# Performance work log

Measured on AMD Instinct MI355X. Metric: run time of the kernel, lower is better.

Reference implementation:

```python
import jax, jax.numpy as jnp
import numpy as np

NUM_HEADS = 16
NUM_KV_HEADS = 4
HEAD_DIM = 128
WINDOW = 1024  # sliding window: key j visible to query i iff 0 <= i - j <= WINDOW
SCALE = 0.08838834764831845  # 1/sqrt(HEAD_DIM)
NEG_INF = -1e30


def setup_inputs() -> dict:
    key = jax.random.key(0)
    k1, k2, k3, k4 = jax.random.split(key, 4)
    B, S = 4, 2048
    T = B * S
    return {
        "q": jax.random.normal(k1, (T, NUM_HEADS * HEAD_DIM), dtype=jnp.float32),
        "k": jax.random.normal(k2, (T, NUM_KV_HEADS * HEAD_DIM), dtype=jnp.float32),
        "v": jax.random.normal(k3, (T, NUM_KV_HEADS * HEAD_DIM), dtype=jnp.float32),
        "sinks": jax.random.normal(k4, (NUM_HEADS,), dtype=jnp.float32),
        "batch": B,
        "seqlen": S,
    }


def reference(q, k, v, sinks, batch, seqlen):
    """Varlen causal sliding-window attention with learnable per-head sink logits.

    Equal-length sequences: total_tokens = batch * seqlen, matching
    cu_seqlens = [0, S, 2S, ...] in flash_attn_varlen_func.
    """
    B, S = batch, seqlen
    g = NUM_HEADS // NUM_KV_HEADS
    q = q.reshape(B, S, NUM_HEADS, HEAD_DIM)
    k = k.reshape(B, S, NUM_KV_HEADS, HEAD_DIM)
    v = v.reshape(B, S, NUM_KV_HEADS, HEAD_DIM)
    # GQA: expand kv heads to match query heads
    k = jnp.repeat(k, g, axis=2)  # [B,S,H,D]
    v = jnp.repeat(v, g, axis=2)

    logits = jnp.einsum("bqhd,bkhd->bhqk", q, k) * SCALE  # [B,H,S,S]

    i = jnp.arange(S)[:, None]
    j = jnp.arange(S)[None, :]
    mask = (j <= i) & ((i - j) <= WINDOW)  # causal + sliding window (left=WINDOW, right=-1)
    logits = jnp.where(mask, logits, NEG_INF)

    # Learnable sink: one extra virtual logit per head, contributing no value.
    sink_col = jnp.broadcast_to(sinks[None, :, None, None], (B, NUM_HEADS, S, 1))
    logits = jnp.concatenate([logits, sink_col], axis=-1)  # [B,H,S,S+1]
    probs = jax.nn.softmax(logits, axis=-1)[..., :S]  # drop sink prob (value = 0)

    o = jnp.einsum("bhqk,bkhd->bqhd", probs, v)  # [B,S,H,D]
    return o.reshape(B * S, NUM_HEADS * HEAD_DIM)
```

## Files before the change

### kernel.cpp

```cpp
#include <hip/hip_runtime.h>
#include <hip/hip_bf16.h>

#define NH    16
#define NKVH  4
#define HD    128
#define WIN   1024
#define SEQ   2048
#define NB    4
#define QROW  (NH * HD)
#define KROW  (NKVH * HD)
#define LOG2E 1.4426950408889634f
#define QSC   (0.08838834764831845f * LOG2E)

#define KSTR 136
#define VSTR 40

typedef __attribute__((ext_vector_type(8))) short short8;
typedef __attribute__((ext_vector_type(4))) float float4v;

__device__ __forceinline__ unsigned short f2bf(float f) {
    unsigned int u = __float_as_uint(f);
    unsigned int r = (u + 0x7FFFu + ((u >> 16) & 1u)) >> 16;
    return (unsigned short)r;
}

__device__ __forceinline__ unsigned int pk2bf(float a, float b) {
    float2 t; t.x = a; t.y = b;
    __hip_bfloat162 h = __float22bfloat162_rn(t);
    union { __hip_bfloat162 h; unsigned int u; } cv;
    cv.h = h;
    return cv.u;
}

__global__ __launch_bounds__(256)
void cvt_k_kernel(const float* __restrict__ kg, unsigned short* __restrict__ kb) {
    const size_t idx = ((size_t)blockIdx.x * 256 + threadIdx.x) * 8;
    float4 a = *(const float4*)(kg + idx);
    float4 b = *(const float4*)(kg + idx + 4);
    uint4 w;
    w.x = pk2bf(a.x, a.y); w.y = pk2bf(a.z, a.w);
    w.z = pk2bf(b.x, b.y); w.w = pk2bf(b.z, b.w);
    *(uint4*)(kb + idx) = w;
}

#define VTSTR 72
__global__ __launch_bounds__(256)
void cvt_vt_kernel(const float* __restrict__ vg, unsigned short* __restrict__ vt) {
    __shared__ unsigned short T[128 * VTSTR];
    const int blk = blockIdx.x;
    const int b   = blk >> 7;
    const int kvh = (blk >> 5) & 3;
    const int kb  = blk & 31;
    const int t   = threadIdx.x;

    const int klocal = t >> 2;
    const int d0     = (t & 3) * 32;
    const float* src = vg + (size_t)(b * SEQ + kb * 64 + klocal) * KROW + kvh * HD + d0;
#pragma unroll
    for (int c = 0; c < 8; ++c) {
        float4 x = *(const float4*)(src + c * 4);
        T[(d0 + c * 4 + 0) * VTSTR + klocal] = f2bf(x.x);
        T[(d0 + c * 4 + 1) * VTSTR + klocal] = f2bf(x.y);
        T[(d0 + c * 4 + 2) * VTSTR + klocal] = f2bf(x.z);
        T[(d0 + c * 4 + 3) * VTSTR + klocal] = f2bf(x.w);
    }
    __syncthreads();

    const int d    = t >> 1;
    const int half = t & 1;
    const unsigned short* s = &T[d * VTSTR + half * 32];
    unsigned short* dst = vt + ((size_t)((b * NKVH + kvh) * HD) + d) * SEQ + kb * 64 + half * 32;
#pragma unroll
    for (int c = 0; c < 4; ++c)
        *(uint4*)(dst + c * 8) = *(const uint4*)(s + c * 8);
}

__global__ __launch_bounds__(256, 3)
void attn_swa_sink_kernel(const float* __restrict__ qg,
                          const unsigned short* __restrict__ kb,
                          const unsigned short* __restrict__ vt,
                          const float* __restrict__ sinks,
                          float* __restrict__ og) {
    __shared__ __align__(16) unsigned short Klds[32 * KSTR];
    __shared__ __align__(16) unsigned short Vlds[128 * VSTR];

    const int gid  = blockIdx.x;
    const int xcd  = gid & 7;
    const int rest = gid >> 3;
    const int qt   = rest >> 1;
    const int g    = ((rest & 1) << 3) | xcd;
    const int b    = g >> 2;
    const int kvh  = g & 3;

    const int tid  = threadIdx.x;
    const int wave = tid >> 6;
    const int lane = tid & 63;
    const int l15  = lane & 15;
    const int quad = lane >> 4;
    const int h    = kvh * 4 + wave;
    const int q0   = qt * 32;

    const float* qbase = qg + (size_t)(b * SEQ) * QROW;
    const unsigned short* kbase = kb + (size_t)(b * SEQ) * KROW + kvh * HD;
    const unsigned short* vtbase = vt + (size_t)((b * NKVH + kvh) * HD) * SEQ;

    short8 qf[2][4];
#pragma unroll
    for (int qs = 0; qs < 2; ++qs) {
        const float* qr = qbase + (size_t)(q0 + qs * 16 + l15) * QROW + h * HD + quad * 8;
#pragma unroll
        for (int c = 0; c < 4; ++c) {
            float4 x = *(const float4*)(qr + c * 32);
            float4 y = *(const float4*)(qr + c * 32 + 4);
            union { unsigned int u[4]; short8 s; } cv;
            cv.u[0] = pk2bf(x.x * QSC, x.y * QSC);
            cv.u[1] = pk2bf(x.z * QSC, x.w * QSC);
            cv.u[2] = pk2bf(y.x * QSC, y.y * QSC);
            cv.u[3] = pk2bf(y.z * QSC, y.w * QSC);
            qf[qs][c] = cv.s;
        }
    }

    const float sinkv = sinks[h] * LOG2E;
    float m_i[2] = { sinkv, sinkv };
    float l_i[2] = { 1.0f, 1.0f };
    float4v accO[2][8];
#pragma unroll
    for (int qs = 0; qs < 2; ++qs)
#pragma unroll
        for (int f = 0; f < 8; ++f) accO[qs][f] = (float4v)0.0f;

    const int kr  = tid >> 3, kcg = tid & 7;
    const int lrow = ((kr & 1) << 4) | (kr >> 1);
    const int vd  = tid >> 1, vh = tid & 1;

    int kt0 = q0 - WIN; if (kt0 < 0) kt0 = 0;
    const int kend = q0 + 32;

    uint4 kpre0, kpre1, vpre0, vpre1;
    {
        const unsigned short* kp = kbase + (size_t)(kt0 + kr) * KROW + kcg * 16;
        kpre0 = *(const uint4*)(kp);
        kpre1 = *(const uint4*)(kp + 8);
        const unsigned short* vp = vtbase + (size_t)vd * SEQ + kt0 + vh * 16;
        vpre0 = *(const uint4*)(vp);
        vpre1 = *(const uint4*)(vp + 8);
    }

    for (int k0 = kt0; k0 < kend; k0 += 32) {
        __syncthreads();
        *(uint4*)&Klds[lrow * KSTR + kcg * 16]     = kpre0;
        *(uint4*)&Klds[lrow * KSTR + kcg * 16 + 8] = kpre1;
        *(uint4*)&Vlds[vd * VSTR + vh * 16]        = vpre0;
        *(uint4*)&Vlds[vd * VSTR + vh * 16 + 8]    = vpre1;
        if (k0 + 32 < kend) {
            const unsigned short* kp = kbase + (size_t)(k0 + 32 + kr) * KROW + kcg * 16;
            kpre0 = *(const uint4*)(kp);
            kpre1 = *(const uint4*)(kp + 8);
            const unsigned short* vp = vtbase + (size_t)vd * SEQ + (k0 + 32) + vh * 16;
            vpre0 = *(const uint4*)(vp);
            vpre1 = *(const uint4*)(vp + 8);
        }
        __syncthreads();

        float4v sacc[2][2];
        sacc[0][0] = (float4v)0.0f; sacc[0][1] = (float4v)0.0f;
        sacc[1][0] = (float4v)0.0f; sacc[1][1] = (float4v)0.0f;
#pragma unroll
        for (int c = 0; c < 4; ++c) {
            short8 kf0 = *(const short8*)&Klds[(l15)      * KSTR + c * 32 + quad * 8];
            short8 kf1 = *(const short8*)&Klds[(16 + l15) * KSTR + c * 32 + quad * 8];
            sacc[0][0] = __builtin_amdgcn_mfma_f32_16x16x32_bf16(kf0, qf[0][c], sacc[0][0], 0, 0, 0);
            sacc[0][1] = __builtin_amdgcn_mfma_f32_16x16x32_bf16(kf0, qf[1][c], sacc[0][1], 0, 0, 0);
            sacc[1][0] = __builtin_amdgcn_mfma_f32_16x16x32_bf16(kf1, qf[0][c], sacc[1][0], 0, 0, 0);
            sacc[1][1] = __builtin_amdgcn_mfma_f32_16x16x32_bf16(kf1, qf[1][c], sacc[1][1], 0, 0, 0);
        }

        short8 pf[2];
#pragma unroll
        for (int qs = 0; qs < 2; ++qs) {
            const int query = q0 + qs * 16 + l15;
            const bool full = (k0 + 31 <= q0 + qs * 16) && (q0 + qs * 16 + 15 - k0 <= WIN);
            float ps[2][4];
            float mx = -3.0e38f;
            if (full) {
#pragma unroll
                for (int ks = 0; ks < 2; ++ks)
#pragma unroll
                    for (int r = 0; r < 4; ++r) {
                        float s = sacc[ks][qs][r];
                        ps[ks][r] = s;
                        mx = fmaxf(mx, s);
                    }
            } else {
#pragma unroll
                for (int ks = 0; ks < 2; ++ks)
#pragma unroll
                    for (int r = 0; r < 4; ++r) {
                        const int key = k0 + 8 * quad + 2 * r + ks;
                        const unsigned d = (unsigned)(query - key);
                        float s = (d <= WIN) ? sacc[ks][qs][r] : -1.0e30f;
                        ps[ks][r] = s;
                        mx = fmaxf(mx, s);
                    }
            }
            mx = fmaxf(mx, __shfl_xor(mx, 16));
            mx = fmaxf(mx, __shfl_xor(mx, 32));
            const float mold = m_i[qs];
            const float mnew = fmaxf(mold, mx);
            m_i[qs] = mnew;
            float sum = 0.0f;
            union { unsigned int u[4]; short8 s; } cv;
#pragma unroll
            for (int r = 0; r < 4; ++r) {
                const float p0 = exp2f(ps[0][r] - mnew);
                const float p1 = exp2f(ps[1][r] - mnew);
                sum += p0 + p1;
                cv.u[r] = pk2bf(p0, p1);
            }
            pf[qs] = cv.s;
            sum += __shfl_xor(sum, 16);
            sum += __shfl_xor(sum, 32);
            if (__any(mnew > mold)) {
                const float alpha = exp2f(mold - mnew);
                l_i[qs] = l_i[qs] * alpha + sum;
#pragma unroll
                for (int r = 0; r < 4; ++r) {
                    const float ar = __shfl(alpha, quad * 4 + r);
#pragma unroll
                    for (int f = 0; f < 8; ++f) accO[qs][f][r] *= ar;
                }
            } else {
                l_i[qs] += sum;
            }
        }

#pragma unroll
        for (int f = 0; f < 8; ++f) {
            short8 vf = *(const short8*)&Vlds[(f * 16 + l15) * VSTR + quad * 8];
            accO[0][f] = __builtin_amdgcn_mfma_f32_16x16x32_bf16(pf[0], vf, accO[0][f], 0, 0, 0);
            accO[1][f] = __builtin_amdgcn_mfma_f32_16x16x32_bf16(pf[1], vf, accO[1][f], 0, 0, 0);
        }
    }

    float* obase = og + (size_t)(b * SEQ) * QROW + h * HD;
#pragma unroll
    for (int qs = 0; qs < 2; ++qs) {
#pragma unroll
        for (int r = 0; r < 4; ++r) {
            const float lq  = __shfl(l_i[qs], quad * 4 + r);
            const float inv = __builtin_amdgcn_rcpf(lq);
            float* orow = obase + (size_t)(q0 + qs * 16 + quad * 4 + r) * QROW;
#pragma unroll
            for (int f = 0; f < 8; ++f)
                orow[f * 16 + l15] = accO[qs][f][r] * inv;
        }
    }
}

extern "C" void kernel_launch(void* const* d_in, const int* in_sizes, int n_in,
                              void* d_out, int out_size, void* d_ws, size_t ws_size,
                              hipStream_t stream) {
    const float* q     = (const float*)d_in[0];
    const float* k     = (const float*)d_in[1];
    const float* v     = (const float*)d_in[2];
    const float* sinks = (const float*)d_in[3];
    float* o = (float*)d_out;

    unsigned short* kb = (unsigned short*)d_ws;
    unsigned short* vt = kb + (size_t)NB * SEQ * KROW;

    cvt_k_kernel<<<dim3(NB * SEQ * KROW / (256 * 8)), dim3(256), 0, stream>>>(k, kb);
    cvt_vt_kernel<<<dim3(NB * NKVH * (SEQ / 64)), dim3(256), 0, stream>>>(v, vt);

    attn_swa_sink_kernel<<<dim3(NB * NKVH * (SEQ / 32)), dim3(256), 0, stream>>>(
        q, kb, vt, sinks, o);
}
```

Baseline: 244.1 us.

## Load K/V fragments directly from global into registers, drop LDS staging

Removes the shared-memory staging of K and V tiles and the two block barriers per iteration. Each wave now loads its MFMA fragments straight from global memory, with K prefetched one tile ahead in registers. The change also lowers the occupancy hint to 2, reverses the q-tile order so the longest tiles launch first, adds s_setprio around the MFMA blocks, and applies lazy max rescaling with a threshold of 8. The cost is that every wave fetches K/V redundantly through cache instead of sharing one LDS copy, and register pressure rises.

```diff
diff --git a/kernel.cpp b/kernel.cpp
--- a/kernel.cpp
+++ b/kernel.cpp
@@ -11,9 +11,7 @@
 #define KROW  (NKVH * HD)
 #define LOG2E 1.4426950408889634f
 #define QSC   (0.08838834764831845f * LOG2E)
-
-#define KSTR 136
-#define VSTR 40
+#define DTHR  8.0f
 
 typedef __attribute__((ext_vector_type(8))) short short8;
 typedef __attribute__((ext_vector_type(4))) float float4v;
@@ -75,19 +73,16 @@
         *(uint4*)(dst + c * 8) = *(const uint4*)(s + c * 8);
 }
 
-__global__ __launch_bounds__(256, 3)
+__global__ __launch_bounds__(256, 2)
 void attn_swa_sink_kernel(const float* __restrict__ qg,
                           const unsigned short* __restrict__ kb,
                           const unsigned short* __restrict__ vt,
                           const float* __restrict__ sinks,
                           float* __restrict__ og) {
-    __shared__ __align__(16) unsigned short Klds[32 * KSTR];
-    __shared__ __align__(16) unsigned short Vlds[128 * VSTR];
-
     const int gid  = blockIdx.x;
     const int xcd  = gid & 7;
     const int rest = gid >> 3;
-    const int qt   = rest >> 1;
+    const int qt   = 63 - (rest >> 1);
     const int g    = ((rest & 1) << 3) | xcd;
     const int b    = g >> 2;
     const int kvh  = g & 3;
@@ -130,50 +125,47 @@
 #pragma unroll
         for (int f = 0; f < 8; ++f) accO[qs][f] = (float4v)0.0f;
 
-    const int kr  = tid >> 3, kcg = tid & 7;
-    const int lrow = ((kr & 1) << 4) | (kr >> 1);
-    const int vd  = tid >> 1, vh = tid & 1;
-
     int kt0 = q0 - WIN; if (kt0 < 0) kt0 = 0;
     const int kend = q0 + 32;
 
-    uint4 kpre0, kpre1, vpre0, vpre1;
-    {
-        const unsigned short* kp = kbase + (size_t)(kt0 + kr) * KROW + kcg * 16;
-        kpre0 = *(const uint4*)(kp);
-        kpre1 = *(const uint4*)(kp + 8);
-        const unsigned short* vp = vtbase + (size_t)vd * SEQ + kt0 + vh * 16;
-        vpre0 = *(const uint4*)(vp);
-        vpre1 = *(const uint4*)(vp + 8);
-    }
+    const unsigned short* kpn = kbase + (size_t)(kt0 + 2 * l15) * KROW + quad * 8;
+    const unsigned short* vp = vtbase + (size_t)l15 * SEQ + kt0 + quad * 8;
+
+    short8 kf[2][4];
+#pragma unroll
+    for (int c = 0; c < 4; ++c) {
+        kf[0][c] = *(const short8*)(kpn + c * 32);
+        kf[1][c] = *(const short8*)(kpn + KROW + c * 32);
+    }
+    kpn += 32 * KROW;
 
     for (int k0 = kt0; k0 < kend; k0 += 32) {
-        __syncthreads();
-        *(uint4*)&Klds[lrow * KSTR + kcg * 16]     = kpre0;
-        *(uint4*)&Klds[lrow * KSTR + kcg * 16 + 8] = kpre1;
-        *(uint4*)&Vlds[vd * VSTR + vh * 16]        = vpre0;
-        *(uint4*)&Vlds[vd * VSTR + vh * 16 + 8]    = vpre1;
-        if (k0 + 32 < kend) {
-            const unsigned short* kp = kbase + (size_t)(k0 + 32 + kr) * KROW + kcg * 16;
-            kpre0 = *(const uint4*)(kp);
-            kpre1 = *(const uint4*)(kp + 8);
-            const unsigned short* vp = vtbase + (size_t)vd * SEQ + (k0 + 32) + vh * 16;
-            vpre0 = *(const uint4*)(vp);
-            vpre1 = *(const uint4*)(vp + 8);
-        }
-        __syncthreads();
+        short8 vf[8];
+#pragma unroll
+        for (int f = 0; f < 8; ++f)
+            vf[f] = *(const short8*)(vp + (size_t)(f * 16) * SEQ);
+        vp += 32;
 
         float4v sacc[2][2];
         sacc[0][0] = (float4v)0.0f; sacc[0][1] = (float4v)0.0f;
         sacc[1][0] = (float4v)0.0f; sacc[1][1] = (float4v)0.0f;
+        __builtin_amdgcn_s_setprio(1);
 #pragma unroll
         for (int c = 0; c < 4; ++c) {
-            short8 kf0 = *(const short8*)&Klds[(l15)      * KSTR + c * 32 + quad * 8];
-            short8 kf1 = *(const short8*)&Klds[(16 + l15) * KSTR + c * 32 + quad * 8];
-            sacc[0][0] = __builtin_amdgcn_mfma_f32_16x16x32_bf16(kf0, qf[0][c], sacc[0][0], 0, 0, 0);
-            sacc[0][1] = __builtin_amdgcn_mfma_f32_16x16x32_bf16(kf0, qf[1][c], sacc[0][1], 0, 0, 0);
-            sacc[1][0] = __builtin_amdgcn_mfma_f32_16x16x32_bf16(kf1, qf[0][c], sacc[1][0], 0, 0, 0);
-            sacc[1][1] = __builtin_amdgcn_mfma_f32_16x16x32_bf16(kf1, qf[1][c], sacc[1][1], 0, 0, 0);
+            sacc[0][0] = __builtin_amdgcn_mfma_f32_16x16x32_bf16(kf[0][c], qf[0][c], sacc[0][0], 0, 0, 0);
+            sacc[0][1] = __builtin_amdgcn_mfma_f32_16x16x32_bf16(kf[0][c], qf[1][c], sacc[0][1], 0, 0, 0);
+            sacc[1][0] = __builtin_amdgcn_mfma_f32_16x16x32_bf16(kf[1][c], qf[0][c], sacc[1][0], 0, 0, 0);
+            sacc[1][1] = __builtin_amdgcn_mfma_f32_16x16x32_bf16(kf[1][c], qf[1][c], sacc[1][1], 0, 0, 0);
+        }
+        __builtin_amdgcn_s_setprio(0);
+
+        if (k0 + 32 < kend) {
+#pragma unroll
+            for (int c = 0; c < 4; ++c) {
+                kf[0][c] = *(const short8*)(kpn + c * 32);
+                kf[1][c] = *(const short8*)(kpn + KROW + c * 32);
+            }
+            kpn += 32 * KROW;
         }
 
         short8 pf[2];
@@ -207,7 +199,9 @@
             mx = fmaxf(mx, __shfl_xor(mx, 16));
             mx = fmaxf(mx, __shfl_xor(mx, 32));
             const float mold = m_i[qs];
-            const float mnew = fmaxf(mold, mx);
+            const bool resc = __any(mx > mold + DTHR);
+            float mnew = mold;
+            if (resc) mnew = fmaxf(mold, mx);
             m_i[qs] = mnew;
             float sum = 0.0f;
             union { unsigned int u[4]; short8 s; } cv;
@@ -221,7 +215,7 @@
             pf[qs] = cv.s;
             sum += __shfl_xor(sum, 16);
             sum += __shfl_xor(sum, 32);
-            if (__any(mnew > mold)) {
+            if (resc) {
                 const float alpha = exp2f(mold - mnew);
                 l_i[qs] = l_i[qs] * alpha + sum;
 #pragma unroll
@@ -235,12 +229,13 @@
             }
         }
 
+        __builtin_amdgcn_s_setprio(1);
 #pragma unroll
         for (int f = 0; f < 8; ++f) {
-            short8 vf = *(const short8*)&Vlds[(f * 16 + l15) * VSTR + quad * 8];
-            accO[0][f] = __builtin_amdgcn_mfma_f32_16x16x32_bf16(pf[0], vf, accO[0][f], 0, 0, 0);
-            accO[1][f] = __builtin_amdgcn_mfma_f32_16x16x32_bf16(pf[1], vf, accO[1][f], 0, 0, 0);
-        }
+            accO[0][f] = __builtin_amdgcn_mfma_f32_16x16x32_bf16(pf[0], vf[f], accO[0][f], 0, 0, 0);
+            accO[1][f] = __builtin_amdgcn_mfma_f32_16x16x32_bf16(pf[1], vf[f], accO[1][f], 0, 0, 0);
+        }
+        __builtin_amdgcn_s_setprio(0);
     }
 
     float* obase = og + (size_t)(b * SEQ) * QROW + h * HD;
```

Measured after the change: 342.8 us. +40.4%, slower.
